# Kernel tuning notes

Measured on AMD Instinct MI355X. Metric: run time of the kernel, lower is better.

Reference implementation:

```python
import jax, jax.numpy as jnp
import numpy as np

B, T, D = 32, 2048, 512

def setup_inputs() -> dict:
    key = jax.random.key(0)
    x = jax.random.normal(key, (B, T, D), dtype=jnp.float32)
    return {"x": x}

def reference(x) -> jnp.ndarray:
    # w[b,t] = sum_s <x_bt, x_bs> - <x_bt, x_bt>
    # Equivalent to x_bt . (sum_s x_bs) - ||x_bt||^2; avoids the [B,T,T] matrix.
    s = x.sum(axis=1)                                  # [B, D]
    w = jnp.einsum('btd,bd->bt', x, s) - (x * x).sum(axis=-1)  # [B, T]
    weights = jax.nn.softmax(w, axis=1)                # softmax over time
    # weighted pooling over time -> [B, D]
    representations = jnp.einsum('btd,bt->bd', x, weights)
    return representations
```

## Files before the change

### kernel.cpp

```cpp
#include <hip/hip_runtime.h>
#include <math.h>

constexpr int B = 32;
constexpr int T = 2048;
constexpr int D = 512;

constexpr int C1 = 32;
constexpr int R1 = T / C1;
constexpr int C2 = 32;
constexpr int R2 = T / C2;
constexpr int NPART = C2 * 4;

__global__ __launch_bounds__(256) void colsum_part(const float* __restrict__ x,
                                                   float* __restrict__ P1) {
    const int b = blockIdx.x, c = blockIdx.y;
    const int d4 = threadIdx.x & 127;
    const int rp = threadIdx.x >> 7;
    const float4* xp = (const float4*)x + ((size_t)(b * T + c * R1) * D >> 2)
                       + (size_t)rp * (D / 4) + d4;
    float4 acc = {0.f, 0.f, 0.f, 0.f};
    #pragma unroll 8
    for (int i = 0; i < R1 / 2; ++i) {
        float4 v = xp[(size_t)i * (D / 2)];
        acc.x += v.x; acc.y += v.y; acc.z += v.z; acc.w += v.w;
    }
    __shared__ float4 lds[128];
    if (rp == 1) lds[d4] = acc;
    __syncthreads();
    if (rp == 0) {
        float4 o = lds[d4];
        acc.x += o.x; acc.y += o.y; acc.z += o.z; acc.w += o.w;
        ((float4*)P1)[(size_t)(b * C1 + c) * (D / 4) + d4] = acc;
    }
}

__global__ __launch_bounds__(256) void online_pool(const float* __restrict__ x,
                                                   const float* __restrict__ P1,
                                                   float* __restrict__ Mp,
                                                   float* __restrict__ Sp,
                                                   float* __restrict__ Op) {
    const int b = blockIdx.x, c = blockIdx.y;
    const int wid = threadIdx.x >> 6, lane = threadIdx.x & 63;

    float4 s0 = {0.f,0.f,0.f,0.f}, s1 = {0.f,0.f,0.f,0.f};
    const float4* pp = (const float4*)P1 + (size_t)b * C1 * (D / 4) + lane * 2;
    #pragma unroll
    for (int k = 0; k < C1; ++k) {
        float4 a = pp[k * (D / 4)], q = pp[k * (D / 4) + 1];
        s0.x += a.x; s0.y += a.y; s0.z += a.z; s0.w += a.w;
        s1.x += q.x; s1.y += q.y; s1.z += q.z; s1.w += q.w;
    }

    float m = -INFINITY, ssum = 0.f;
    float4 O0 = {0.f,0.f,0.f,0.f}, O1 = {0.f,0.f,0.f,0.f};
    const int t0 = c * R2 + wid * (R2 / 4);
    const float4* xr = (const float4*)x + ((size_t)(b * T + t0) * D >> 2) + lane * 2;

    #pragma unroll 2
    for (int i = 0; i < R2 / 4; ++i) {
        float4 x0 = xr[0], x1 = xr[1];
        xr += D / 4;
        float a;
        a =      x0.x * (s0.x - x0.x);
        a = fmaf(x0.y,  s0.y - x0.y, a);
        a = fmaf(x0.z,  s0.z - x0.z, a);
        a = fmaf(x0.w,  s0.w - x0.w, a);
        a = fmaf(x1.x,  s1.x - x1.x, a);
        a = fmaf(x1.y,  s1.y - x1.y, a);
        a = fmaf(x1.z,  s1.z - x1.z, a);
        a = fmaf(x1.w,  s1.w - x1.w, a);
        #pragma unroll
        for (int off = 1; off < 64; off <<= 1)
            a += __shfl_xor(a, off, 64);
        const float wr = a;
        if (wr <= m) {
            const float e = __expf(wr - m);
            ssum += e;
            O0.x = fmaf(e, x0.x, O0.x); O0.y = fmaf(e, x0.y, O0.y);
            O0.z = fmaf(e, x0.z, O0.z); O0.w = fmaf(e, x0.w, O0.w);
            O1.x = fmaf(e, x1.x, O1.x); O1.y = fmaf(e, x1.y, O1.y);
            O1.z = fmaf(e, x1.z, O1.z); O1.w = fmaf(e, x1.w, O1.w);
        } else {
            const float al = __expf(m - wr);
            ssum = fmaf(ssum, al, 1.f);
            O0.x = fmaf(O0.x, al, x0.x); O0.y = fmaf(O0.y, al, x0.y);
            O0.z = fmaf(O0.z, al, x0.z); O0.w = fmaf(O0.w, al, x0.w);
            O1.x = fmaf(O1.x, al, x1.x); O1.y = fmaf(O1.y, al, x1.y);
            O1.z = fmaf(O1.z, al, x1.z); O1.w = fmaf(O1.w, al, x1.w);
            m = wr;
        }
    }

    const int pi = (b * C2 + c) * 4 + wid;
    if (lane == 0) { Mp[pi] = m; Sp[pi] = ssum; }
    float4* op = (float4*)Op + (size_t)pi * (D / 4) + lane * 2;
    op[0] = O0; op[1] = O1;
}

__global__ __launch_bounds__(128) void finalize(const float* __restrict__ Mp,
                                                const float* __restrict__ Sp,
                                                const float* __restrict__ Op,
                                                float* __restrict__ out) {
    const int b = blockIdx.x, tid = threadIdx.x;
    const int wid = tid >> 6;
    __shared__ float fsh[NPART];
    __shared__ float red[2];

    const float Mc = Mp[b * NPART + tid];
    float m = Mc;
    #pragma unroll
    for (int off = 1; off < 64; off <<= 1) m = fmaxf(m, __shfl_xor(m, off, 64));
    if ((tid & 63) == 0) red[wid] = m;
    __syncthreads();
    const float Mg = fmaxf(red[0], red[1]);
    __syncthreads();

    const float f = __expf(Mc - Mg);
    fsh[tid] = f;
    float sp = Sp[b * NPART + tid] * f;
    #pragma unroll
    for (int off = 1; off < 64; off <<= 1) sp += __shfl_xor(sp, off, 64);
    if ((tid & 63) == 0) red[wid] = sp;
    __syncthreads();
    const float Sg = red[0] + red[1];

    float4 acc = {0.f,0.f,0.f,0.f};
    const float4* op = (const float4*)Op + (size_t)b * NPART * (D / 4) + tid;
    #pragma unroll 4
    for (int c = 0; c < NPART; ++c) {
        const float fc = fsh[c];
        float4 v = op[(size_t)c * (D / 4)];
        acc.x = fmaf(fc, v.x, acc.x); acc.y = fmaf(fc, v.y, acc.y);
        acc.z = fmaf(fc, v.z, acc.z); acc.w = fmaf(fc, v.w, acc.w);
    }
    const float inv = 1.0f / Sg;
    acc.x *= inv; acc.y *= inv; acc.z *= inv; acc.w *= inv;
    ((float4*)out)[(size_t)b * (D / 4) + tid] = acc;
}

extern "C" void kernel_launch(void* const* d_in, const int* in_sizes, int n_in,
                              void* d_out, int out_size, void* d_ws, size_t ws_size,
                              hipStream_t stream) {
    const float* x = (const float*)d_in[0];
    float* out = (float*)d_out;

    float* P1 = (float*)d_ws;
    float* Mp = P1 + (size_t)B * C1 * D;
    float* Sp = Mp + (size_t)B * NPART;
    float* Op = Sp + (size_t)B * NPART;

    colsum_part<<<dim3(B, C1), 256, 0, stream>>>(x, P1);
    online_pool<<<dim3(B, C2), 256, 0, stream>>>(x, P1, Mp, Sp, Op);
    finalize<<<B, 128, 0, stream>>>(Mp, Sp, Op, out);
}
```

Measured before the change: 234.8 us.

## Batch row loads per wave, split column-sum reduction, parallelize final merge with atomics

The column-sum partials are now reduced once per batch in a new small kernel, instead of every pool block re-summing 32 partials. The pool kernel now has each wave load 8 rows up front into registers. It computes the 8 logits, reduces them with interleaved shuffles and does a local softmax. This replaces the serial, branchy online-softmax loop and exposes more memory-level parallelism across twice as many blocks. The final merge is spread over 8 blocks per batch that accumulate into a zeroed output with atomicAdd. The cost is an extra kernel launch, twice the partial-output traffic, float atomics with non-deterministic summation order, and higher register pressure.

```diff
diff --git a/kernel.cpp b/kernel.cpp
--- a/kernel.cpp
+++ b/kernel.cpp
@@ -7,8 +7,8 @@
 
 constexpr int C1 = 32;
 constexpr int R1 = T / C1;
-constexpr int C2 = 32;
-constexpr int R2 = T / C2;
+constexpr int C2 = 64;
+constexpr int RW = 8;
 constexpr int NPART = C2 * 4;
 
 __global__ __launch_bounds__(256) void colsum_part(const float* __restrict__ x,
@@ -34,61 +34,86 @@
     }
 }
 
-__global__ __launch_bounds__(256) void online_pool(const float* __restrict__ x,
-                                                   const float* __restrict__ P1,
-                                                   float* __restrict__ Mp,
-                                                   float* __restrict__ Sp,
-                                                   float* __restrict__ Op) {
+__global__ __launch_bounds__(256) void reduce_s(const float* __restrict__ P1,
+                                                float* __restrict__ s,
+                                                float* __restrict__ out) {
+    const int b = blockIdx.x;
+    const int d4 = threadIdx.x & 127, half = threadIdx.x >> 7;
+    const float4* pp = (const float4*)P1 + ((size_t)b * C1 + half * (C1 / 2)) * (D / 4) + d4;
+    float4 acc = {0.f, 0.f, 0.f, 0.f};
+    #pragma unroll
+    for (int k = 0; k < C1 / 2; ++k) {
+        float4 v = pp[(size_t)k * (D / 4)];
+        acc.x += v.x; acc.y += v.y; acc.z += v.z; acc.w += v.w;
+    }
+    __shared__ float4 lds[128];
+    if (half == 1) {
+        lds[d4] = acc;
+        ((float4*)out)[(size_t)b * (D / 4) + d4] = make_float4(0.f, 0.f, 0.f, 0.f);
+    }
+    __syncthreads();
+    if (half == 0) {
+        float4 o = lds[d4];
+        acc.x += o.x; acc.y += o.y; acc.z += o.z; acc.w += o.w;
+        ((float4*)s)[(size_t)b * (D / 4) + d4] = acc;
+    }
+}
+
+__global__ __launch_bounds__(256) void fused_pool(const float* __restrict__ x,
+                                                  const float* __restrict__ s,
+                                                  float* __restrict__ Mp,
+                                                  float* __restrict__ Sp,
+                                                  float* __restrict__ Op) {
     const int b = blockIdx.x, c = blockIdx.y;
     const int wid = threadIdx.x >> 6, lane = threadIdx.x & 63;
 
-    float4 s0 = {0.f,0.f,0.f,0.f}, s1 = {0.f,0.f,0.f,0.f};
-    const float4* pp = (const float4*)P1 + (size_t)b * C1 * (D / 4) + lane * 2;
+    const float4* sp4 = (const float4*)(s + (size_t)b * D) + lane * 2;
+    const float4 s0 = sp4[0], s1 = sp4[1];
+
+    const int t0 = c * (RW * 4) + wid * RW;
+    const float4* xr = (const float4*)(x + ((size_t)b * T + t0) * D) + lane * 2;
+
+    float4 X0[RW], X1[RW];
     #pragma unroll
-    for (int k = 0; k < C1; ++k) {
-        float4 a = pp[k * (D / 4)], q = pp[k * (D / 4) + 1];
-        s0.x += a.x; s0.y += a.y; s0.z += a.z; s0.w += a.w;
-        s1.x += q.x; s1.y += q.y; s1.z += q.z; s1.w += q.w;
+    for (int r = 0; r < RW; ++r) {
+        X0[r] = xr[0]; X1[r] = xr[1];
+        xr += D / 4;
+    }
+    float a[RW];
+    #pragma unroll
+    for (int r = 0; r < RW; ++r) {
+        float t;
+        t =      X0[r].x * (s0.x - X0[r].x);
+        t = fmaf(X0[r].y,  s0.y - X0[r].y, t);
+        t = fmaf(X0[r].z,  s0.z - X0[r].z, t);
+        t = fmaf(X0[r].w,  s0.w - X0[r].w, t);
+        t = fmaf(X1[r].x,  s1.x - X1[r].x, t);
+        t = fmaf(X1[r].y,  s1.y - X1[r].y, t);
+        t = fmaf(X1[r].z,  s1.z - X1[r].z, t);
+        t = fmaf(X1[r].w,  s1.w - X1[r].w, t);
+        a[r] = t;
     }
 
-    float m = -INFINITY, ssum = 0.f;
+    #pragma unroll
+    for (int off = 1; off < 64; off <<= 1) {
+        #pragma unroll
+        for (int r = 0; r < RW; ++r)
+            a[r] += __shfl_xor(a[r], off, 64);
+    }
+
+    float m = fmaxf(fmaxf(fmaxf(a[0], a[1]), fmaxf(a[2], a[3])),
+                    fmaxf(fmaxf(a[4], a[5]), fmaxf(a[6], a[7])));
+    float e[RW], ssum = 0.f;
+    #pragma unroll
+    for (int r = 0; r < RW; ++r) { e[r] = __expf(a[r] - m); ssum += e[r]; }
+
     float4 O0 = {0.f,0.f,0.f,0.f}, O1 = {0.f,0.f,0.f,0.f};
-    const int t0 = c * R2 + wid * (R2 / 4);
-    const float4* xr = (const float4*)x + ((size_t)(b * T + t0) * D >> 2) + lane * 2;
-
-    #pragma unroll 2
-    for (int i = 0; i < R2 / 4; ++i) {
-        float4 x0 = xr[0], x1 = xr[1];
-        xr += D / 4;
-        float a;
-        a =      x0.x * (s0.x - x0.x);
-        a = fmaf(x0.y,  s0.y - x0.y, a);
-        a = fmaf(x0.z,  s0.z - x0.z, a);
-        a = fmaf(x0.w,  s0.w - x0.w, a);
-        a = fmaf(x1.x,  s1.x - x1.x, a);
-        a = fmaf(x1.y,  s1.y - x1.y, a);
-        a = fmaf(x1.z,  s1.z - x1.z, a);
-        a = fmaf(x1.w,  s1.w - x1.w, a);
-        #pragma unroll
-        for (int off = 1; off < 64; off <<= 1)
-            a += __shfl_xor(a, off, 64);
-        const float wr = a;
-        if (wr <= m) {
-            const float e = __expf(wr - m);
-            ssum += e;
-            O0.x = fmaf(e, x0.x, O0.x); O0.y = fmaf(e, x0.y, O0.y);
-            O0.z = fmaf(e, x0.z, O0.z); O0.w = fmaf(e, x0.w, O0.w);
-            O1.x = fmaf(e, x1.x, O1.x); O1.y = fmaf(e, x1.y, O1.y);
-            O1.z = fmaf(e, x1.z, O1.z); O1.w = fmaf(e, x1.w, O1.w);
-        } else {
-            const float al = __expf(m - wr);
-            ssum = fmaf(ssum, al, 1.f);
-            O0.x = fmaf(O0.x, al, x0.x); O0.y = fmaf(O0.y, al, x0.y);
-            O0.z = fmaf(O0.z, al, x0.z); O0.w = fmaf(O0.w, al, x0.w);
-            O1.x = fmaf(O1.x, al, x1.x); O1.y = fmaf(O1.y, al, x1.y);
-            O1.z = fmaf(O1.z, al, x1.z); O1.w = fmaf(O1.w, al, x1.w);
-            m = wr;
-        }
+    #pragma unroll
+    for (int r = 0; r < RW; ++r) {
+        O0.x = fmaf(e[r], X0[r].x, O0.x); O0.y = fmaf(e[r], X0[r].y, O0.y);
+        O0.z = fmaf(e[r], X0[r].z, O0.z); O0.w = fmaf(e[r], X0[r].w, O0.w);
+        O1.x = fmaf(e[r], X1[r].x, O1.x); O1.y = fmaf(e[r], X1[r].y, O1.y);
+        O1.z = fmaf(e[r], X1[r].z, O1.z); O1.w = fmaf(e[r], X1[r].w, O1.w);
     }
 
     const int pi = (b * C2 + c) * 4 + wid;
@@ -97,45 +122,50 @@
     op[0] = O0; op[1] = O1;
 }
 
-__global__ __launch_bounds__(128) void finalize(const float* __restrict__ Mp,
-                                                const float* __restrict__ Sp,
-                                                const float* __restrict__ Op,
-                                                float* __restrict__ out) {
-    const int b = blockIdx.x, tid = threadIdx.x;
-    const int wid = tid >> 6;
+__global__ __launch_bounds__(256) void merge_out(const float* __restrict__ Mp,
+                                                 const float* __restrict__ Sp,
+                                                 const float* __restrict__ Op,
+                                                 float* __restrict__ out) {
+    const int b = blockIdx.x, j = blockIdx.y;
+    const int tid = threadIdx.x, wid = tid >> 6, lane = tid & 63;
     __shared__ float fsh[NPART];
-    __shared__ float red[2];
+    __shared__ float red[4];
 
     const float Mc = Mp[b * NPART + tid];
     float m = Mc;
     #pragma unroll
     for (int off = 1; off < 64; off <<= 1) m = fmaxf(m, __shfl_xor(m, off, 64));
-    if ((tid & 63) == 0) red[wid] = m;
+    if (lane == 0) red[wid] = m;
     __syncthreads();
-    const float Mg = fmaxf(red[0], red[1]);
+    const float Mg = fmaxf(fmaxf(red[0], red[1]), fmaxf(red[2], red[3]));
     __syncthreads();
 
     const float f = __expf(Mc - Mg);
     fsh[tid] = f;
-    float sp = Sp[b * NPART + tid] * f;
+    float spv = Sp[b * NPART + tid] * f;
     #pragma unroll
-    for (int off = 1; off < 64; off <<= 1) sp += __shfl_xor(sp, off, 64);
-    if ((tid & 63) == 0) red[wid] = sp;
+    for (int off = 1; off < 64; off <<= 1) spv += __shfl_xor(spv, off, 64);
+    if (lane == 0) red[wid] = spv;
     __syncthreads();
-    const float Sg = red[0] + red[1];
+    const float Sg = red[0] + red[1] + red[2] + red[3];
+    const float inv = 1.0f / Sg;
 
+    const int d4 = tid & 127, pr = tid >> 7;
+    const int p0 = j * 32 + pr * 16;
     float4 acc = {0.f,0.f,0.f,0.f};
-    const float4* op = (const float4*)Op + (size_t)b * NPART * (D / 4) + tid;
+    const float4* op = (const float4*)Op + ((size_t)b * NPART + p0) * (D / 4) + d4;
     #pragma unroll 4
-    for (int c = 0; c < NPART; ++c) {
-        const float fc = fsh[c];
-        float4 v = op[(size_t)c * (D / 4)];
+    for (int i = 0; i < 16; ++i) {
+        const float fc = fsh[p0 + i];
+        float4 v = op[(size_t)i * (D / 4)];
         acc.x = fmaf(fc, v.x, acc.x); acc.y = fmaf(fc, v.y, acc.y);
         acc.z = fmaf(fc, v.z, acc.z); acc.w = fmaf(fc, v.w, acc.w);
     }
-    const float inv = 1.0f / Sg;
-    acc.x *= inv; acc.y *= inv; acc.z *= inv; acc.w *= inv;
-    ((float4*)out)[(size_t)b * (D / 4) + tid] = acc;
+    float* o = out + (size_t)b * D + d4 * 4;
+    atomicAdd(o + 0, acc.x * inv);
+    atomicAdd(o + 1, acc.y * inv);
+    atomicAdd(o + 2, acc.z * inv);
+    atomicAdd(o + 3, acc.w * inv);
 }
 
 extern "C" void kernel_launch(void* const* d_in, const int* in_sizes, int n_in,
@@ -145,11 +175,13 @@
     float* out = (float*)d_out;
 
     float* P1 = (float*)d_ws;
-    float* Mp = P1 + (size_t)B * C1 * D;
+    float* s  = P1 + (size_t)B * C1 * D;
+    float* Mp = s + (size_t)B * D;
     float* Sp = Mp + (size_t)B * NPART;
     float* Op = Sp + (size_t)B * NPART;
 
     colsum_part<<<dim3(B, C1), 256, 0, stream>>>(x, P1);
-    online_pool<<<dim3(B, C2), 256, 0, stream>>>(x, P1, Mp, Sp, Op);
-    finalize<<<B, 128, 0, stream>>>(Mp, Sp, Op, out);
+    reduce_s<<<B, 256, 0, stream>>>(P1, s, out);
+    fused_pool<<<dim3(B, C2), 256, 0, stream>>>(x, s, Mp, Sp, Op);
+    merge_out<<<dim3(B, 8), 256, 0, stream>>>(Mp, Sp, Op, out);
 }
```

Result: faster. 225.1 us (-4.1%).
